# Performance work log

Hardware: AMD Instinct MI355X
Metric: run time of the kernel (lower is better)

## Reference

```python
import jax, jax.numpy as jnp
import numpy as np

C = 512  # channels

def _maxpool2x2(x):
    # x: [B,H,W,C] -> [B,H/2,W/2,C]
    B, H, W, Cc = x.shape
    return x.reshape(B, H // 2, 2, W // 2, 2, Cc).max(axis=(2, 4))

def setup_inputs() -> dict:
    key = jax.random.key(0)
    ks = jax.random.split(key, 6)
    x = jax.random.normal(ks[0], (16, 64, 64, C), dtype=jnp.float32)
    # 1x1 conv kernels stored as [C_in, C_out]; spectral norm treated as identity
    # on the (already-normalized) effective weights.
    s = lambda k, i, o: jax.random.normal(k, (i, o), dtype=jnp.float32) / np.sqrt(i)
    W_theta = s(ks[1], C, C // 8)
    W_phi = s(ks[2], C, C // 8)
    W_g = s(ks[3], C, C // 2)
    W_o = s(ks[4], C // 2, C)
    gamma = jnp.float32(0.7)  # nonzero so the attention path matters
    return {"x": x, "W_theta": W_theta, "W_phi": W_phi, "W_g": W_g,
            "W_o": W_o, "gamma": gamma}

def reference(x, W_theta, W_phi, W_g, W_o, gamma):
    B, H, W, Cc = x.shape
    S = H * W            # query length
    Sk = S // 4          # key/value length after 2x2 maxpool
    theta = jnp.einsum('bhwc,cd->bhwd', x, W_theta)              # [B,H,W,C/8]
    phi = _maxpool2x2(jnp.einsum('bhwc,cd->bhwd', x, W_phi))     # [B,H/2,W/2,C/8]
    g = _maxpool2x2(jnp.einsum('bhwc,cd->bhwd', x, W_g))         # [B,H/2,W/2,C/2]
    theta = theta.reshape(B, S, Cc // 8)
    phi = phi.reshape(B, Sk, Cc // 8)
    g = g.reshape(B, Sk, Cc // 2)
    # scores [B,S,Sk]; SAGAN omits the 1/sqrt(d_k) scaling
    beta = jax.nn.softmax(jnp.einsum('bqd,bkd->bqk', theta, phi), axis=-1)
    tmp = jnp.einsum('bqk,bkv->bqv', beta, g).reshape(B, H, W, Cc // 2)
    o = jnp.einsum('bhwv,vc->bhwc', tmp, W_o)
    return gamma * o + x
```

## Files before the change

kernel.cpp:

```cpp
#include <hip/hip_runtime.h>

typedef __attribute__((ext_vector_type(8))) short bf16x8;
typedef __attribute__((ext_vector_type(4))) float f32x4;
typedef unsigned short u16;
typedef unsigned int u32;

#define MFMA __builtin_amdgcn_mfma_f32_16x16x32_bf16

static __device__ __forceinline__ float b2f(u16 u) {
    u32 x = ((u32)u) << 16;
    return __builtin_bit_cast(float, x);
}
static __device__ __forceinline__ u16 f2b(float f) {
    u32 u = __builtin_bit_cast(u32, f);
    u32 r = (u + 0x7fffu + ((u >> 16) & 1u)) >> 16;
    return (u16)r;
}
static __device__ __forceinline__ void async16(const u16* g, u16* l) {
    __builtin_amdgcn_global_load_lds(
        (const __attribute__((address_space(1))) u32*)g,
        (__attribute__((address_space(3))) u32*)l, 16, 0, 0);
}

__global__ __launch_bounds__(256) void xcast(const float* __restrict__ x, u16* __restrict__ xb) {
    size_t i = ((size_t)blockIdx.x * 256 + threadIdx.x) * 8;
    f32x4 f0 = *(const f32x4*)(x + i);
    f32x4 f1 = *(const f32x4*)(x + i + 4);
    bf16x8 v;
    v[0] = (short)f2b(f0[0]); v[1] = (short)f2b(f0[1]);
    v[2] = (short)f2b(f0[2]); v[3] = (short)f2b(f0[3]);
    v[4] = (short)f2b(f1[0]); v[5] = (short)f2b(f1[1]);
    v[6] = (short)f2b(f1[2]); v[7] = (short)f2b(f1[3]);
    *(bf16x8*)(xb + i) = v;
}

__global__ void pack_w(const float* __restrict__ Wt, const float* __restrict__ Wp,
                       const float* __restrict__ Wg, const float* __restrict__ Wo,
                       u16* __restrict__ WcatT, u16* __restrict__ WoT) {
    int t = blockIdx.x * 256 + threadIdx.x;
    const int n1 = 384 * 512;
    if (t < n1) {
        int n = t >> 9, k = t & 511;
        float v;
        if (n < 64)       v = Wt[k * 64 + n];
        else if (n < 128) v = Wp[k * 64 + (n - 64)];
        else              v = Wg[k * 256 + (n - 128)];
        WcatT[t] = f2b(v);
    } else {
        int j = t - n1;
        if (j < 512 * 256) {
            int n = j >> 8, k = j & 255;
            WoT[j] = f2b(Wo[k * 512 + n]);
        }
    }
}

template <int K>
static __device__ __forceinline__ void gemm_core(const u16* __restrict__ A,
                                                 const u16* __restrict__ Bt,
                                                 int m0, int n0, int lda, int ldb,
                                                 f32x4 acc[4][4], u16* As, u16* Bs) {
    const int t = threadIdx.x;
    const int w = t >> 6, li = t & 15, quad = (t >> 4) & 3;
    const int wm = (w & 1) << 6, wn = (w >> 1) << 6;
#pragma unroll
    for (int mi = 0; mi < 4; mi++)
#pragma unroll
        for (int ni = 0; ni < 4; ni++) acc[mi][ni] = (f32x4)0.0f;
    const u16* ag = A + (size_t)(m0 + (t >> 2)) * lda + ((t & 3) << 3);
    const u16* bg = Bt + (size_t)(n0 + (t >> 2)) * ldb + ((t & 3) << 3);
    u16* asw = As + w * 512;
    u16* bsw = Bs + w * 512;
    for (int k0 = 0; k0 < K; k0 += 32) {
        __syncthreads();
        async16(ag + k0, asw);
        async16(ag + k0 + (size_t)64 * lda, asw + 2048);
        async16(bg + k0, bsw);
        async16(bg + k0 + (size_t)64 * ldb, bsw + 2048);
        __syncthreads();
        bf16x8 af[4], bfr[4];
#pragma unroll
        for (int mi = 0; mi < 4; mi++)
            af[mi] = *(const bf16x8*)(As + (wm + mi * 16 + li) * 32 + quad * 8);
#pragma unroll
        for (int ni = 0; ni < 4; ni++)
            bfr[ni] = *(const bf16x8*)(Bs + (wn + ni * 16 + li) * 32 + quad * 8);
#pragma unroll
        for (int mi = 0; mi < 4; mi++)
#pragma unroll
            for (int ni = 0; ni < 4; ni++)
                acc[mi][ni] = MFMA(af[mi], bfr[ni], acc[mi][ni], 0, 0, 0);
    }
    __syncthreads();
}

static __device__ __forceinline__ void epi_bf16(const f32x4 acc[4][4], u16* ebuf,
                                                u16* __restrict__ outp, int ld,
                                                int row0, int col0) {
    const int t = threadIdx.x;
    const int li = t & 15, quad = (t >> 4) & 3;
#pragma unroll
    for (int mi = 0; mi < 4; mi++)
#pragma unroll
        for (int ni = 0; ni < 4; ni++)
#pragma unroll
            for (int r = 0; r < 4; r++)
                ebuf[(mi * 16 + quad * 4 + r) * 72 + ni * 16 + li] = f2b(acc[mi][ni][r]);
    const int rr = (t & 63) >> 3, cc = (t & 7) * 8;
#pragma unroll
    for (int j = 0; j < 8; j++) {
        int row = j * 8 + rr;
        bf16x8 v = *(const bf16x8*)(ebuf + row * 72 + cc);
        *(bf16x8*)(outp + (size_t)(row0 + row) * ld + col0 + cc) = v;
    }
}

__global__ __launch_bounds__(256) void proj_gemm(const u16* __restrict__ xb,
                                                 const u16* __restrict__ WcatT,
                                                 u16* __restrict__ theta,
                                                 u16* __restrict__ ppg) {
    __shared__ __attribute__((aligned(16))) u16 sbuf[18432];
    u16* As = sbuf;
    u16* Bs = sbuf + 4096;
    int bm = blockIdx.x / 3, bn = blockIdx.x % 3;
    f32x4 acc[4][4];
    gemm_core<512>(xb, WcatT, bm * 128, bn * 128, 512, 512, acc, As, Bs);
    const int w = threadIdx.x >> 6;
    u16* ebuf = sbuf + w * 4608;
    int row0 = bm * 128 + (w & 1) * 64;
    int gcol = bn * 128 + (w >> 1) * 64;
    if (gcol < 64) epi_bf16(acc, ebuf, theta, 64, row0, 0);
    else           epi_bf16(acc, ebuf, ppg, 320, row0, gcol - 64);
}

__global__ void pool_phi(const u16* __restrict__ ppg, u16* __restrict__ phi) {
    int t = blockIdx.x * 256 + threadIdx.x;
    int c = t & 63;
    int pos = (t >> 6) & 1023;
    int b = t >> 16;
    int h2 = pos >> 5, w2 = pos & 31;
    size_t base = ((size_t)(b << 12) + h2 * 128 + w2 * 2) * 320 + c;
    float v0 = b2f(ppg[base]), v1 = b2f(ppg[base + 320]);
    float v2 = b2f(ppg[base + 320 * 64]), v3 = b2f(ppg[base + 320 * 65]);
    float m = fmaxf(fmaxf(v0, v1), fmaxf(v2, v3));
    phi[((size_t)(b << 10) + pos) * 64 + c] = f2b(m);
}

__global__ void pool_gt(const u16* __restrict__ ppg, u16* __restrict__ gT) {
    __shared__ float tile[64][65];
    int bid = blockIdx.x;
    int b = bid >> 6;
    int rem = bid & 63;
    int c0 = (rem >> 4) * 64;
    int pos0 = (rem & 15) * 64;
    int t = threadIdx.x;
#pragma unroll
    for (int i = 0; i < 16; i++) {
        int o = t + i * 256;
        int cl = o & 63, pl = o >> 6;
        int pos = pos0 + pl;
        int h2 = pos >> 5, w2 = pos & 31;
        size_t base = ((size_t)(b << 12) + h2 * 128 + w2 * 2) * 320 + 64 + c0 + cl;
        float v0 = b2f(ppg[base]), v1 = b2f(ppg[base + 320]);
        float v2 = b2f(ppg[base + 320 * 64]), v3 = b2f(ppg[base + 320 * 65]);
        tile[pl][cl] = fmaxf(fmaxf(v0, v1), fmaxf(v2, v3));
    }
    __syncthreads();
    int cl = t >> 2, ch = t & 3;
    u16 valbuf[16] __attribute__((aligned(16)));
#pragma unroll
    for (int j = 0; j < 16; j++) valbuf[j] = f2b(tile[ch * 16 + j][cl]);
    u16* dst = gT + ((size_t)b * 256 + c0 + cl) * 1024 + pos0 + ch * 16;
    *(uint4*)(dst) = *(const uint4*)(valbuf);
    *(uint4*)(dst + 8) = *(const uint4*)(valbuf + 8);
}

__global__ __launch_bounds__(256, 3) void attn_fused(const u16* __restrict__ theta,
                                                     const u16* __restrict__ phi,
                                                     const u16* __restrict__ gT,
                                                     u16* __restrict__ tmp) {
    __shared__ __attribute__((aligned(16))) u16 lds[24576];
    u16* stgP = lds;
    u16* stgG = lds + 4096;
    u16* pbuf = lds + 20480;

    int bid = blockIdx.x;
    int swz = (bid & 7) * 128 + (bid >> 3);
    int b = swz >> 6;
    int q0 = (swz & 63) << 6;
    const int t = threadIdx.x;
    const int w = t >> 6, li = t & 15, quad = (t >> 4) & 3;

    const u16* thp = theta + (((size_t)(b << 12) + q0 + w * 16 + li) << 6) + quad * 8;
    bf16x8 tq0 = *(const bf16x8*)thp;
    bf16x8 tq1 = *(const bf16x8*)(thp + 32);

    const int srow = t >> 3;
    const int sc = (t & 7) ^ (srow & 7);
    const u16* phisrc = phi + ((size_t)(b << 10) + srow) * 64 + sc * 8;
    const u16* gsrc = gT + ((size_t)(b << 8) + srow) * 1024 + sc * 8;
    u16* pb = pbuf + w * 1024;

    f32x4 o[16];
#pragma unroll
    for (int ni = 0; ni < 16; ni++) o[ni] = (f32x4)0.0f;
    float m = -3.0e38f, sum = 0.0f;

    for (int kc = 0; kc < 16; kc++) {
        __syncthreads();
        async16(phisrc + (size_t)(kc * 64) * 64, stgP + w * 512);
        async16(phisrc + (size_t)(kc * 64 + 32) * 64, stgP + 2048 + w * 512);
#pragma unroll
        for (int j = 0; j < 8; j++)
            async16(gsrc + (size_t)(j * 32) * 1024 + kc * 64, stgG + j * 2048 + w * 512);
        __syncthreads();

        f32x4 sacc[4];
#pragma unroll
        for (int nf = 0; nf < 4; nf++) sacc[nf] = (f32x4)0.0f;
#pragma unroll
        for (int nf = 0; nf < 4; nf++) {
            int row = nf * 16 + li;
            int p0 = quad ^ (li & 7);
            int p1 = (4 + quad) ^ (li & 7);
            bf16x8 f0 = *(const bf16x8*)(stgP + row * 64 + p0 * 8);
            bf16x8 f1 = *(const bf16x8*)(stgP + row * 64 + p1 * 8);
            sacc[nf] = MFMA(f0, tq0, sacc[nf], 0, 0, 0);
            sacc[nf] = MFMA(f1, tq1, sacc[nf], 0, 0, 0);
        }

        float mc = sacc[0][0];
#pragma unroll
        for (int nf = 0; nf < 4; nf++)
#pragma unroll
            for (int r = 0; r < 4; r++) mc = fmaxf(mc, sacc[nf][r]);
        mc = fmaxf(mc, __shfl_xor(mc, 16, 64));
        mc = fmaxf(mc, __shfl_xor(mc, 32, 64));
        if (!__all(mc <= m + 8.0f)) {
            float nm = fmaxf(m, mc);
            float f = __expf(m - nm);
            sum *= f;
#pragma unroll
            for (int ni = 0; ni < 16; ni++)
#pragma unroll
                for (int r = 0; r < 4; r++) o[ni][r] *= f;
            m = nm;
        }
        float p[16];
        float s = 0.0f;
#pragma unroll
        for (int nf = 0; nf < 4; nf++)
#pragma unroll
            for (int r = 0; r < 4; r++) {
                float e = __expf(sacc[nf][r] - m);
                p[nf * 4 + r] = e;
                s += e;
            }
        s += __shfl_xor(s, 16, 64);
        s += __shfl_xor(s, 32, 64);
        sum += s;

#pragma unroll
        for (int nf = 0; nf < 4; nf++) {
            int cc = nf * 2 + (quad >> 1);
            int pos = cc ^ (li & 7);
            u32* dst = (u32*)(pb + li * 64 + pos * 8 + (quad & 1) * 4);
            dst[0] = (u32)f2b(p[nf * 4 + 0]) | ((u32)f2b(p[nf * 4 + 1]) << 16);
            dst[1] = (u32)f2b(p[nf * 4 + 2]) | ((u32)f2b(p[nf * 4 + 3]) << 16);
        }

#pragma unroll
        for (int w2 = 0; w2 < 2; w2++) {
            int pos8 = ((w2 * 4 + quad) ^ (li & 7)) * 8;
            bf16x8 pf = *(const bf16x8*)(pb + li * 64 + pos8);
#pragma unroll
            for (int ni = 0; ni < 16; ni++) {
                bf16x8 gf = *(const bf16x8*)(stgG + (ni * 16 + li) * 64 + pos8);
                o[ni] = MFMA(gf, pf, o[ni], 0, 0, 0);
            }
        }
    }

    float inv = 1.0f / sum;
#pragma unroll
    for (int ni = 0; ni < 16; ni++)
#pragma unroll
        for (int r = 0; r < 4; r++) o[ni][r] *= inv;

    __syncthreads();
    u16* eb = lds + w * 4224;
#pragma unroll
    for (int ni = 0; ni < 16; ni++) {
        u32* d = (u32*)(eb + li * 264 + ni * 16 + quad * 4);
        d[0] = (u32)f2b(o[ni][0]) | ((u32)f2b(o[ni][1]) << 16);
        d[1] = (u32)f2b(o[ni][2]) | ((u32)f2b(o[ni][3]) << 16);
    }
    const int lane = t & 63;
#pragma unroll
    for (int pss = 0; pss < 8; pss++) {
        int row = pss * 2 + (lane >> 5);
        bf16x8 v = *(const bf16x8*)(eb + row * 264 + (lane & 31) * 8);
        *(bf16x8*)(tmp + ((size_t)(b << 12) + q0 + w * 16 + row) * 256 + (lane & 31) * 8) = v;
    }
}

__global__ __launch_bounds__(256) void out_gemm(const u16* __restrict__ tmp,
                                                const u16* __restrict__ WoT,
                                                const float* __restrict__ x,
                                                const float* __restrict__ gamma_p,
                                                float* __restrict__ out) {
    __shared__ __attribute__((aligned(16))) u16 sbuf[18432];
    u16* As = sbuf;
    u16* Bs = sbuf + 4096;
    int bm = blockIdx.x >> 2, bn = blockIdx.x & 3;
    f32x4 acc[4][4];
    gemm_core<256>(tmp, WoT, bm * 128, bn * 128, 256, 256, acc, As, Bs);
    float gamma = gamma_p[0];
    const int t = threadIdx.x;
    const int w = t >> 6, li = t & 15, quad = (t >> 4) & 3;
    int row0 = bm * 128 + (w & 1) * 64;
    int col0 = bn * 128 + (w >> 1) * 64;
    float* fb = (float*)sbuf + w * 2176;
    const int rr = (t & 63) >> 4, ccv = (t & 15) * 4;
#pragma unroll
    for (int half = 0; half < 2; half++) {
#pragma unroll
        for (int mi = 0; mi < 2; mi++)
#pragma unroll
            for (int ni = 0; ni < 4; ni++)
#pragma unroll
                for (int r = 0; r < 4; r++)
                    fb[(mi * 16 + quad * 4 + r) * 68 + ni * 16 + li] =
                        acc[half * 2 + mi][ni][r];
#pragma unroll
        for (int j = 0; j < 8; j++) {
            int row = j * 4 + rr;
            f32x4 v = *(const f32x4*)(fb + row * 68 + ccv);
            size_t go = (size_t)(row0 + half * 32 + row) * 512 + col0 + ccv;
            f32x4 xv = *(const f32x4*)(x + go);
#pragma unroll
            for (int e = 0; e < 4; e++) v[e] = gamma * v[e] + xv[e];
            *(f32x4*)(out + go) = v;
        }
    }
}

extern "C" void kernel_launch(void* const* d_in, const int* in_sizes, int n_in,
                              void* d_out, int out_size, void* d_ws, size_t ws_size,
                              hipStream_t stream) {
    (void)in_sizes; (void)n_in; (void)out_size; (void)ws_size;
    const float* x  = (const float*)d_in[0];
    const float* Wt = (const float*)d_in[1];
    const float* Wp = (const float*)d_in[2];
    const float* Wg = (const float*)d_in[3];
    const float* Wo = (const float*)d_in[4];
    const float* gm = (const float*)d_in[5];
    float* out = (float*)d_out;

    char* ws = (char*)d_ws;
    size_t off = 0;
    u16* WcatT = (u16*)(ws + off); off += (size_t)384 * 512 * 2;
    u16* WoT   = (u16*)(ws + off); off += (size_t)512 * 256 * 2;
    u16* xb    = (u16*)(ws + off); off += (size_t)65536 * 512 * 2;
    u16* theta = (u16*)(ws + off); off += (size_t)65536 * 64 * 2;
    u16* ppg   = (u16*)(ws + off); off += (size_t)65536 * 320 * 2;
    u16* phi = xb;
    u16* gT  = xb + (size_t)16 * 1024 * 64;
    u16* tmp = ppg;

    pack_w<<<1280, 256, 0, stream>>>(Wt, Wp, Wg, Wo, WcatT, WoT);
    xcast<<<16384, 256, 0, stream>>>(x, xb);
    proj_gemm<<<1536, 256, 0, stream>>>(xb, WcatT, theta, ppg);
    pool_phi<<<4096, 256, 0, stream>>>(ppg, phi);
    pool_gt<<<1024, 256, 0, stream>>>(ppg, gT);
    attn_fused<<<1024, 256, 0, stream>>>(theta, phi, gT, tmp);
    out_gemm<<<2048, 256, 0, stream>>>(tmp, WoT, x, gm, out);
}
```

Before: 426.2 us.

## Process two query groups per wave in attention to reuse staged K/V tiles

Each attention block now covers 128 queries instead of 64, and each wave handles two 16-query groups. The phi and gT tiles staged in LDS are reused across both groups, which halves global K/V traffic per query and the number of staging barriers per unit of work. The grid drops to 512 blocks, and the doubled accumulators raise register pressure, so launch bounds go from 3 to 2 blocks per CU. The P buffer LDS region also grows. The risk is lower occupancy and fewer blocks (512 on 256 CUs) limiting latency hiding.

```diff
diff --git a/kernel.cpp b/kernel.cpp
--- a/kernel.cpp
+++ b/kernel.cpp
@@ -175,36 +175,41 @@
     *(uint4*)(dst + 8) = *(const uint4*)(valbuf + 8);
 }
 
-__global__ __launch_bounds__(256, 3) void attn_fused(const u16* __restrict__ theta,
+__global__ __launch_bounds__(256, 2) void attn_fused(const u16* __restrict__ theta,
                                                      const u16* __restrict__ phi,
                                                      const u16* __restrict__ gT,
                                                      u16* __restrict__ tmp) {
-    __shared__ __attribute__((aligned(16))) u16 lds[24576];
+    __shared__ __attribute__((aligned(16))) u16 lds[28672];
     u16* stgP = lds;
     u16* stgG = lds + 4096;
     u16* pbuf = lds + 20480;
 
     int bid = blockIdx.x;
-    int swz = (bid & 7) * 128 + (bid >> 3);
-    int b = swz >> 6;
-    int q0 = (swz & 63) << 6;
+    int swz = (bid & 7) * 64 + (bid >> 3);
+    int b = swz >> 5;
+    int q0 = (swz & 31) << 7;
     const int t = threadIdx.x;
     const int w = t >> 6, li = t & 15, quad = (t >> 4) & 3;
 
-    const u16* thp = theta + (((size_t)(b << 12) + q0 + w * 16 + li) << 6) + quad * 8;
-    bf16x8 tq0 = *(const bf16x8*)thp;
-    bf16x8 tq1 = *(const bf16x8*)(thp + 32);
+    const u16* thp = theta + (((size_t)(b << 12) + q0 + w * 32 + li) << 6) + quad * 8;
+    bf16x8 tq[2][2];
+    tq[0][0] = *(const bf16x8*)thp;
+    tq[0][1] = *(const bf16x8*)(thp + 32);
+    tq[1][0] = *(const bf16x8*)(thp + (16 << 6));
+    tq[1][1] = *(const bf16x8*)(thp + (16 << 6) + 32);
 
     const int srow = t >> 3;
     const int sc = (t & 7) ^ (srow & 7);
     const u16* phisrc = phi + ((size_t)(b << 10) + srow) * 64 + sc * 8;
     const u16* gsrc = gT + ((size_t)(b << 8) + srow) * 1024 + sc * 8;
-    u16* pb = pbuf + w * 1024;
-
-    f32x4 o[16];
-#pragma unroll
-    for (int ni = 0; ni < 16; ni++) o[ni] = (f32x4)0.0f;
-    float m = -3.0e38f, sum = 0.0f;
+    u16* pbq[2] = {pbuf + (w * 2 + 0) * 1024, pbuf + (w * 2 + 1) * 1024};
+
+    f32x4 o[2][16];
+#pragma unroll
+    for (int qg = 0; qg < 2; qg++)
+#pragma unroll
+        for (int ni = 0; ni < 16; ni++) o[qg][ni] = (f32x4)0.0f;
+    float m[2] = {-3.0e38f, -3.0e38f}, sum[2] = {0.0f, 0.0f};
 
     for (int kc = 0; kc < 16; kc++) {
         __syncthreads();
@@ -215,9 +220,11 @@
             async16(gsrc + (size_t)(j * 32) * 1024 + kc * 64, stgG + j * 2048 + w * 512);
         __syncthreads();
 
-        f32x4 sacc[4];
-#pragma unroll
-        for (int nf = 0; nf < 4; nf++) sacc[nf] = (f32x4)0.0f;
+        f32x4 sacc[2][4];
+#pragma unroll
+        for (int qg = 0; qg < 2; qg++)
+#pragma unroll
+            for (int nf = 0; nf < 4; nf++) sacc[qg][nf] = (f32x4)0.0f;
 #pragma unroll
         for (int nf = 0; nf < 4; nf++) {
             int row = nf * 16 + li;
@@ -225,82 +232,96 @@
             int p1 = (4 + quad) ^ (li & 7);
             bf16x8 f0 = *(const bf16x8*)(stgP + row * 64 + p0 * 8);
             bf16x8 f1 = *(const bf16x8*)(stgP + row * 64 + p1 * 8);
-            sacc[nf] = MFMA(f0, tq0, sacc[nf], 0, 0, 0);
-            sacc[nf] = MFMA(f1, tq1, sacc[nf], 0, 0, 0);
-        }
-
-        float mc = sacc[0][0];
-#pragma unroll
-        for (int nf = 0; nf < 4; nf++)
-#pragma unroll
-            for (int r = 0; r < 4; r++) mc = fmaxf(mc, sacc[nf][r]);
-        mc = fmaxf(mc, __shfl_xor(mc, 16, 64));
-        mc = fmaxf(mc, __shfl_xor(mc, 32, 64));
-        if (!__all(mc <= m + 8.0f)) {
-            float nm = fmaxf(m, mc);
-            float f = __expf(m - nm);
-            sum *= f;
-#pragma unroll
-            for (int ni = 0; ni < 16; ni++)
-#pragma unroll
-                for (int r = 0; r < 4; r++) o[ni][r] *= f;
-            m = nm;
-        }
-        float p[16];
-        float s = 0.0f;
-#pragma unroll
-        for (int nf = 0; nf < 4; nf++)
-#pragma unroll
-            for (int r = 0; r < 4; r++) {
-                float e = __expf(sacc[nf][r] - m);
-                p[nf * 4 + r] = e;
-                s += e;
+            sacc[0][nf] = MFMA(f0, tq[0][0], sacc[0][nf], 0, 0, 0);
+            sacc[0][nf] = MFMA(f1, tq[0][1], sacc[0][nf], 0, 0, 0);
+            sacc[1][nf] = MFMA(f0, tq[1][0], sacc[1][nf], 0, 0, 0);
+            sacc[1][nf] = MFMA(f1, tq[1][1], sacc[1][nf], 0, 0, 0);
+        }
+
+#pragma unroll
+        for (int qg = 0; qg < 2; qg++) {
+            float mc = sacc[qg][0][0];
+#pragma unroll
+            for (int nf = 0; nf < 4; nf++)
+#pragma unroll
+                for (int r = 0; r < 4; r++) mc = fmaxf(mc, sacc[qg][nf][r]);
+            mc = fmaxf(mc, __shfl_xor(mc, 16, 64));
+            mc = fmaxf(mc, __shfl_xor(mc, 32, 64));
+            if (!__all(mc <= m[qg] + 8.0f)) {
+                float nm = fmaxf(m[qg], mc);
+                float f = __expf(m[qg] - nm);
+                sum[qg] *= f;
+#pragma unroll
+                for (int ni = 0; ni < 16; ni++)
+#pragma unroll
+                    for (int r = 0; r < 4; r++) o[qg][ni][r] *= f;
+                m[qg] = nm;
             }
-        s += __shfl_xor(s, 16, 64);
-        s += __shfl_xor(s, 32, 64);
-        sum += s;
-
-#pragma unroll
-        for (int nf = 0; nf < 4; nf++) {
-            int cc = nf * 2 + (quad >> 1);
-            int pos = cc ^ (li & 7);
-            u32* dst = (u32*)(pb + li * 64 + pos * 8 + (quad & 1) * 4);
-            dst[0] = (u32)f2b(p[nf * 4 + 0]) | ((u32)f2b(p[nf * 4 + 1]) << 16);
-            dst[1] = (u32)f2b(p[nf * 4 + 2]) | ((u32)f2b(p[nf * 4 + 3]) << 16);
+            float p[16];
+            float s = 0.0f;
+#pragma unroll
+            for (int nf = 0; nf < 4; nf++)
+#pragma unroll
+                for (int r = 0; r < 4; r++) {
+                    float e = __expf(sacc[qg][nf][r] - m[qg]);
+                    p[nf * 4 + r] = e;
+                    s += e;
+                }
+            s += __shfl_xor(s, 16, 64);
+            s += __shfl_xor(s, 32, 64);
+            sum[qg] += s;
+
+            u16* pb = pbq[qg];
+#pragma unroll
+            for (int nf = 0; nf < 4; nf++) {
+                int cc = nf * 2 + (quad >> 1);
+                int pos = cc ^ (li & 7);
+                u32* dst = (u32*)(pb + li * 64 + pos * 8 + (quad & 1) * 4);
+                dst[0] = (u32)f2b(p[nf * 4 + 0]) | ((u32)f2b(p[nf * 4 + 1]) << 16);
+                dst[1] = (u32)f2b(p[nf * 4 + 2]) | ((u32)f2b(p[nf * 4 + 3]) << 16);
+            }
         }
 
 #pragma unroll
         for (int w2 = 0; w2 < 2; w2++) {
             int pos8 = ((w2 * 4 + quad) ^ (li & 7)) * 8;
-            bf16x8 pf = *(const bf16x8*)(pb + li * 64 + pos8);
+            bf16x8 pf0 = *(const bf16x8*)(pbq[0] + li * 64 + pos8);
+            bf16x8 pf1 = *(const bf16x8*)(pbq[1] + li * 64 + pos8);
 #pragma unroll
             for (int ni = 0; ni < 16; ni++) {
                 bf16x8 gf = *(const bf16x8*)(stgG + (ni * 16 + li) * 64 + pos8);
-                o[ni] = MFMA(gf, pf, o[ni], 0, 0, 0);
+                o[0][ni] = MFMA(gf, pf0, o[0][ni], 0, 0, 0);
+                o[1][ni] = MFMA(gf, pf1, o[1][ni], 0, 0, 0);
             }
         }
     }
 
-    float inv = 1.0f / sum;
-#pragma unroll
-    for (int ni = 0; ni < 16; ni++)
-#pragma unroll
-        for (int r = 0; r < 4; r++) o[ni][r] *= inv;
+    float inv[2] = {1.0f / sum[0], 1.0f / sum[1]};
+#pragma unroll
+    for (int qg = 0; qg < 2; qg++)
+#pragma unroll
+        for (int ni = 0; ni < 16; ni++)
+#pragma unroll
+            for (int r = 0; r < 4; r++) o[qg][ni][r] *= inv[qg];
 
     __syncthreads();
     u16* eb = lds + w * 4224;
-#pragma unroll
-    for (int ni = 0; ni < 16; ni++) {
-        u32* d = (u32*)(eb + li * 264 + ni * 16 + quad * 4);
-        d[0] = (u32)f2b(o[ni][0]) | ((u32)f2b(o[ni][1]) << 16);
-        d[1] = (u32)f2b(o[ni][2]) | ((u32)f2b(o[ni][3]) << 16);
-    }
     const int lane = t & 63;
 #pragma unroll
-    for (int pss = 0; pss < 8; pss++) {
-        int row = pss * 2 + (lane >> 5);
-        bf16x8 v = *(const bf16x8*)(eb + row * 264 + (lane & 31) * 8);
-        *(bf16x8*)(tmp + ((size_t)(b << 12) + q0 + w * 16 + row) * 256 + (lane & 31) * 8) = v;
+    for (int qg = 0; qg < 2; qg++) {
+#pragma unroll
+        for (int ni = 0; ni < 16; ni++) {
+            u32* d = (u32*)(eb + li * 264 + ni * 16 + quad * 4);
+            d[0] = (u32)f2b(o[qg][ni][0]) | ((u32)f2b(o[qg][ni][1]) << 16);
+            d[1] = (u32)f2b(o[qg][ni][2]) | ((u32)f2b(o[qg][ni][3]) << 16);
+        }
+#pragma unroll
+        for (int pss = 0; pss < 8; pss++) {
+            int row = pss * 2 + (lane >> 5);
+            bf16x8 v = *(const bf16x8*)(eb + row * 264 + (lane & 31) * 8);
+            *(bf16x8*)(tmp + ((size_t)(b << 12) + q0 + w * 32 + qg * 16 + row) * 256 +
+                       (lane & 31) * 8) = v;
+        }
     }
 }
 
@@ -373,6 +394,6 @@
     proj_gemm<<<1536, 256, 0, stream>>>(xb, WcatT, theta, ppg);
     pool_phi<<<4096, 256, 0, stream>>>(ppg, phi);
     pool_gt<<<1024, 256, 0, stream>>>(ppg, gT);
-    attn_fused<<<1024, 256, 0, stream>>>(theta, phi, gT, tmp);
+    attn_fused<<<512, 256, 0, stream>>>(theta, phi, gT, tmp);
     out_gemm<<<2048, 256, 0, stream>>>(tmp, WoT, x, gm, out);
 }
```

Result: faster. 410.5 us (-3.7%).
